# Kernel optimization log

Measured on AMD Instinct MI355X. Metric: run time of the kernel, lower is better.

The kernel has to match this reference:

```python
import jax, jax.numpy as jnp
import numpy as np

N_NODES = 50000
N_EDGES = 800000
N_GRAPHS = 64
IN_DIM, HID_DIM, OUT_DIM = 64, 128, 3


def setup_inputs() -> dict:
    key = jax.random.key(0)
    ks = jax.random.split(key, 8)
    x = jax.random.normal(ks[0], (N_NODES, IN_DIM), dtype=jnp.float32)
    edge_index = jax.random.randint(ks[1], (2, N_EDGES), 0, N_NODES, dtype=jnp.int64)
    batch = jnp.sort(jax.random.randint(ks[2], (N_NODES,), 0, N_GRAPHS, dtype=jnp.int64))
    # Glorot-ish init for weights, zero biases (matches GCNConv/Linear defaults in spirit)
    W1 = jax.random.normal(ks[3], (IN_DIM, HID_DIM), dtype=jnp.float32) / np.sqrt(IN_DIM)
    b1 = jnp.zeros((HID_DIM,), dtype=jnp.float32)
    W2 = jax.random.normal(ks[4], (HID_DIM, HID_DIM), dtype=jnp.float32) / np.sqrt(HID_DIM)
    b2 = jnp.zeros((HID_DIM,), dtype=jnp.float32)
    Wf = jax.random.normal(ks[5], (HID_DIM, OUT_DIM), dtype=jnp.float32) / np.sqrt(HID_DIM)
    bf = jnp.zeros((OUT_DIM,), dtype=jnp.float32)
    return {"x": x, "edge_index": edge_index, "batch": batch,
            "W1": W1, "b1": b1, "W2": W2, "b2": b2, "Wf": Wf, "bf": bf}


def _gcn_conv(x, src, dst, norm, W, b, n_nodes):
    # PyG GCNConv: h = X W; out_i = sum_{j->i} norm_ij * h_j + b
    h = x @ W                                  # [N, D_out]
    msg = h[src] * norm[:, None]               # gather + scale  [E+N, D_out]
    out = jax.ops.segment_sum(msg, dst, num_segments=n_nodes)  # scatter-add
    return out + b


def reference(x, edge_index, batch, W1, b1, W2, b2, Wf, bf):
    n_nodes = x.shape[0]
    loops = jnp.arange(n_nodes, dtype=edge_index.dtype)
    src = jnp.concatenate([edge_index[0], loops])  # add self-loops
    dst = jnp.concatenate([edge_index[1], loops])
    # Symmetric normalization: deg over destinations (incl. self-loops)
    deg = jax.ops.segment_sum(jnp.ones_like(dst, dtype=x.dtype), dst, num_segments=n_nodes)
    dinv = jax.lax.rsqrt(jnp.maximum(deg, 1.0))
    norm = dinv[src] * dinv[dst]               # [E+N]

    h = jax.nn.relu(_gcn_conv(x, src, dst, norm, W1, b1, n_nodes))
    h = jax.nn.relu(_gcn_conv(h, src, dst, norm, W2, b2, n_nodes))

    # global_mean_pool over batch ids
    sums = jax.ops.segment_sum(h, batch, num_segments=N_GRAPHS)        # [G, H]
    counts = jax.ops.segment_sum(jnp.ones((n_nodes,), h.dtype), batch, num_segments=N_GRAPHS)
    pooled = sums / jnp.maximum(counts, 1.0)[:, None]

    return pooled @ Wf + bf                    # [G, OUT_DIM]
```

## Files before the change

kernel.cpp:

```cpp
#include <hip/hip_runtime.h>

constexpr int NN = 50000;
constexpr int NE = 800000;
constexpr int NG = 64;
constexpr int DI = 64;
constexpr int DH = 128;
constexpr int DO = 3;

constexpr int SCAN_B = 256;
constexpr int NBK = 196;
constexpr int CHUNK = 4096;
constexpr int NCH = (NE + CHUNK - 1) / CHUNK;
constexpr int BBTOT = NBK * NCH;
constexpr int NBB = (BBTOT + 255) / 256;

typedef unsigned int u32;

__device__ inline float blo(u32 u) { return __uint_as_float(u << 16); }
__device__ inline float bhi(u32 u) { return __uint_as_float(u & 0xffff0000u); }
__device__ inline u32 f2b(float f) {
    u32 u = __float_as_uint(f);
    return (u + 0x7fffu + ((u >> 16) & 1u)) >> 16;
}
__device__ inline void fma8(float w, uint4 v, float acc[8]) {
    acc[0] = fmaf(w, blo(v.x), acc[0]); acc[1] = fmaf(w, bhi(v.x), acc[1]);
    acc[2] = fmaf(w, blo(v.y), acc[2]); acc[3] = fmaf(w, bhi(v.y), acc[3]);
    acc[4] = fmaf(w, blo(v.z), acc[4]); acc[5] = fmaf(w, bhi(v.z), acc[5]);
    acc[6] = fmaf(w, blo(v.w), acc[6]); acc[7] = fmaf(w, bhi(v.w), acc[7]);
}

__global__ void k_init(const float* __restrict__ x, uint4* __restrict__ xb,
                       float* __restrict__ pooled, const int* __restrict__ batch,
                       int* __restrict__ gstart) {
    int i = blockIdx.x * blockDim.x + threadIdx.x;
    if (i < NN * DI / 8) {
        float4 a = reinterpret_cast<const float4*>(x)[i * 2];
        float4 b = reinterpret_cast<const float4*>(x)[i * 2 + 1];
        uint4 o;
        o.x = f2b(a.x) | (f2b(a.y) << 16);
        o.y = f2b(a.z) | (f2b(a.w) << 16);
        o.z = f2b(b.x) | (f2b(b.y) << 16);
        o.w = f2b(b.z) | (f2b(b.w) << 16);
        xb[i] = o;
    }
    if (i < NG * DH) pooled[i] = 0.0f;
    if (blockIdx.x == 0 && threadIdx.x <= NG) {
        int g = threadIdx.x;
        int lo = 0, hi = NN;
        while (lo < hi) {
            int mid = (lo + hi) >> 1;
            if (batch[mid] < g) lo = mid + 1; else hi = mid;
        }
        gstart[g] = lo;
    }
}

__global__ __launch_bounds__(256) void k_histc(const int* __restrict__ dst,
                                               int* __restrict__ cntBB) {
    __shared__ int lcnt[NBK];
    const int t = threadIdx.x, c = blockIdx.x;
    for (int b = t; b < NBK; b += 256) lcnt[b] = 0;
    __syncthreads();
    const int base = c * CHUNK;
    const int endE = min(base + CHUNK, NE);
    for (int e = base + t; e < endE; e += 256) atomicAdd(&lcnt[dst[e] >> 8], 1);
    __syncthreads();
    for (int b = t; b < NBK; b += 256) cntBB[b * NCH + c] = lcnt[b];
}

__device__ inline void blockScan(int* sm) {
    for (int off = 1; off < SCAN_B; off <<= 1) {
        int add = (threadIdx.x >= off) ? sm[threadIdx.x - off] : 0;
        __syncthreads();
        sm[threadIdx.x] += add;
        __syncthreads();
    }
}

__global__ void k_scanBB1(int* __restrict__ cntBB, int* __restrict__ bbpartial) {
    __shared__ int sm[SCAN_B];
    int i = blockIdx.x * SCAN_B + threadIdx.x;
    int v = (i < BBTOT) ? cntBB[i] : 0;
    sm[threadIdx.x] = v;
    __syncthreads();
    blockScan(sm);
    if (i < BBTOT) cntBB[i] = sm[threadIdx.x] - v;
    if (threadIdx.x == SCAN_B - 1) bbpartial[blockIdx.x] = sm[SCAN_B - 1];
}

__global__ void k_scanB(int* __restrict__ bbpartial) {
    __shared__ int sm[SCAN_B];
    int v = (threadIdx.x < NBB) ? bbpartial[threadIdx.x] : 0;
    sm[threadIdx.x] = v;
    __syncthreads();
    blockScan(sm);
    if (threadIdx.x < NBB) bbpartial[threadIdx.x] = sm[threadIdx.x] - v;
}

__global__ __launch_bounds__(256) void k_fillP2(const int* __restrict__ src,
                                                const int* __restrict__ dst,
                                                const int* __restrict__ cntBB,
                                                const int* __restrict__ bbpartial,
                                                u32* __restrict__ stage) {
    __shared__ int lcur[NBK];
    const int t = threadIdx.x, c = blockIdx.x;
    for (int b = t; b < NBK; b += 256) {
        int i = b * NCH + c;
        lcur[b] = cntBB[i] + bbpartial[i >> 8];
    }
    __syncthreads();
    const int base = c * CHUNK;
    const int endE = min(base + CHUNK, NE);
    for (int e = base + t; e < endE; e += 256) {
        int s = src[e], d = dst[e];
        int slot = atomicAdd(&lcur[d >> 8], 1);
        stage[slot] = ((u32)(d & 255) << 16) | (u32)s;
    }
}

__global__ __launch_bounds__(256) void k_fillB(const u32* __restrict__ stage,
                                               const int* __restrict__ cntBB,
                                               const int* __restrict__ bbpartial,
                                               int* __restrict__ rowptr,
                                               float* __restrict__ dinv,
                                               ushort* __restrict__ csr16) {
    __shared__ int cnt[256];
    __shared__ int sm[256];
    __shared__ int cur[256];
    const int b = blockIdx.x, t = threadIdx.x;
    cnt[t] = 0;
    const int i0 = b * NCH;
    const int beg = cntBB[i0] + bbpartial[i0 >> 8];
    const int end = (b + 1 < NBK) ? cntBB[i0 + NCH] + bbpartial[(i0 + NCH) >> 8] : NE;
    __syncthreads();
    for (int i = beg + t; i < end; i += 256) atomicAdd(&cnt[(stage[i] >> 16) & 255u], 1);
    __syncthreads();
    const int v = cnt[t];
    sm[t] = v;
    __syncthreads();
    blockScan(sm);
    const int excl = sm[t] - v;
    const int n = b * 256 + t;
    if (n < NN) {
        rowptr[n] = beg + excl;
        dinv[n] = rsqrtf((float)(v + 1));
    }
    if (b == NBK - 1 && t == 0) rowptr[NN] = NE;
    cur[t] = beg + excl;
    __syncthreads();
    for (int i = beg + t; i < end; i += 256) {
        u32 e = stage[i];
        int slot = atomicAdd(&cur[(e >> 16) & 255u], 1);
        csr16[slot] = (ushort)(e & 0xffffu);
    }
}

template <int D, bool BIAS_RELU>
__global__ __launch_bounds__(256) void k_agge(const ushort* __restrict__ hb,
                                              const ushort* __restrict__ csr16,
                                              const int* __restrict__ rowptr,
                                              const float* __restrict__ dinv,
                                              const float* __restrict__ bias,
                                              u32* __restrict__ out) {
    constexpr int SUB = D / 8;
    constexpr int NPB = 256 / SUB;
    const int sub = threadIdx.x / SUB;
    const int sl = threadIdx.x % SUB;
    const int node = blockIdx.x * NPB + sub;
    if (node >= NN) return;

    const float dn = dinv[node];
    float acc[8];
    {
        uint4 v = *reinterpret_cast<const uint4*>(hb + (size_t)node * D + sl * 8);
        float w = dn * dn;
        acc[0] = w * blo(v.x); acc[1] = w * bhi(v.x);
        acc[2] = w * blo(v.y); acc[3] = w * bhi(v.y);
        acc[4] = w * blo(v.z); acc[5] = w * bhi(v.z);
        acc[6] = w * blo(v.w); acc[7] = w * bhi(v.w);
    }
    int j = rowptr[node];
    const int end = rowptr[node + 1];
    while ((j & 3) && j < end) {
        int s = csr16[j];
        uint4 g = *reinterpret_cast<const uint4*>(hb + (size_t)s * D + sl * 8);
        fma8(dn * dinv[s], g, acc);
        ++j;
    }
    for (; j + 4 <= end; j += 4) {
        ushort4 q = *reinterpret_cast<const ushort4*>(csr16 + j);
        uint4 g0 = *reinterpret_cast<const uint4*>(hb + (size_t)q.x * D + sl * 8);
        uint4 g1 = *reinterpret_cast<const uint4*>(hb + (size_t)q.y * D + sl * 8);
        uint4 g2 = *reinterpret_cast<const uint4*>(hb + (size_t)q.z * D + sl * 8);
        uint4 g3 = *reinterpret_cast<const uint4*>(hb + (size_t)q.w * D + sl * 8);
        float w0 = dn * dinv[q.x], w1 = dn * dinv[q.y];
        float w2 = dn * dinv[q.z], w3 = dn * dinv[q.w];
        fma8(w0, g0, acc);
        fma8(w1, g1, acc);
        fma8(w2, g2, acc);
        fma8(w3, g3, acc);
    }
    while (j < end) {
        int s = csr16[j];
        uint4 g = *reinterpret_cast<const uint4*>(hb + (size_t)s * D + sl * 8);
        fma8(dn * dinv[s], g, acc);
        ++j;
    }
    if (BIAS_RELU) {
        float4 b0 = *reinterpret_cast<const float4*>(bias + sl * 8);
        float4 b1v = *reinterpret_cast<const float4*>(bias + sl * 8 + 4);
        acc[0] = fmaxf(acc[0] + b0.x, 0.f); acc[1] = fmaxf(acc[1] + b0.y, 0.f);
        acc[2] = fmaxf(acc[2] + b0.z, 0.f); acc[3] = fmaxf(acc[3] + b0.w, 0.f);
        acc[4] = fmaxf(acc[4] + b1v.x, 0.f); acc[5] = fmaxf(acc[5] + b1v.y, 0.f);
        acc[6] = fmaxf(acc[6] + b1v.z, 0.f); acc[7] = fmaxf(acc[7] + b1v.w, 0.f);
    }
    uint4 o;
    o.x = f2b(acc[0]) | (f2b(acc[1]) << 16);
    o.y = f2b(acc[2]) | (f2b(acc[3]) << 16);
    o.z = f2b(acc[4]) | (f2b(acc[5]) << 16);
    o.w = f2b(acc[6]) | (f2b(acc[7]) << 16);
    *reinterpret_cast<uint4*>(reinterpret_cast<ushort*>(out) + (size_t)node * D + sl * 8) = o;
}

__device__ inline float4 fmaf4(float s, float4 w, float4 a) {
    a.x = fmaf(s, w.x, a.x); a.y = fmaf(s, w.y, a.y);
    a.z = fmaf(s, w.z, a.z); a.w = fmaf(s, w.w, a.w);
    return a;
}

constexpr int GR = 32;

__global__ __launch_bounds__(256) void k_gemm12(const ushort* __restrict__ A,
                                                const float* __restrict__ W1,
                                                const float* __restrict__ b1,
                                                const float* __restrict__ W2,
                                                u32* __restrict__ T) {
    constexpr int ASTR = 72;
    __shared__ ushort sU16[GR * DH];
    const int t = threadIdx.x;
    const int row0 = blockIdx.x * GR;
    const int cg = t & 31;
    const int rw = t >> 5;

    {
        const int row = t >> 3;
        const int q = t & 7;
        int gr = row0 + row;
        uint4 v = make_uint4(0u, 0u, 0u, 0u);
        if (gr < NN)
            v = *reinterpret_cast<const uint4*>(A + (size_t)gr * DI + q * 8);
        *reinterpret_cast<uint4*>(&sU16[row * ASTR + q * 8]) = v;
    }
    __syncthreads();

    const float* W1c = W1 + cg * 4;
    float4 acc[4];
#pragma unroll
    for (int j = 0; j < 4; ++j) acc[j] = make_float4(0.f, 0.f, 0.f, 0.f);

#pragma unroll 4
    for (int kk = 0; kk < DI; kk += 4) {
        float4 w0 = *reinterpret_cast<const float4*>(W1c + (kk + 0) * DH);
        float4 w1 = *reinterpret_cast<const float4*>(W1c + (kk + 1) * DH);
        float4 w2 = *reinterpret_cast<const float4*>(W1c + (kk + 2) * DH);
        float4 w3 = *reinterpret_cast<const float4*>(W1c + (kk + 3) * DH);
#pragma unroll
        for (int j = 0; j < 4; ++j) {
            uint2 av = *reinterpret_cast<const uint2*>(&sU16[(rw * 4 + j) * ASTR + kk]);
            acc[j] = fmaf4(blo(av.x), w0, acc[j]);
            acc[j] = fmaf4(bhi(av.x), w1, acc[j]);
            acc[j] = fmaf4(blo(av.y), w2, acc[j]);
            acc[j] = fmaf4(bhi(av.y), w3, acc[j]);
        }
    }
    {
        float4 bb = *reinterpret_cast<const float4*>(b1 + cg * 4);
#pragma unroll
        for (int j = 0; j < 4; ++j) {
            acc[j].x = fmaxf(acc[j].x + bb.x, 0.f);
            acc[j].y = fmaxf(acc[j].y + bb.y, 0.f);
            acc[j].z = fmaxf(acc[j].z + bb.z, 0.f);
            acc[j].w = fmaxf(acc[j].w + bb.w, 0.f);
        }
    }

    __syncthreads();
#pragma unroll
    for (int j = 0; j < 4; ++j) {
        uint2 o = make_uint2(f2b(acc[j].x) | (f2b(acc[j].y) << 16),
                             f2b(acc[j].z) | (f2b(acc[j].w) << 16));
        *reinterpret_cast<uint2*>(&sU16[(rw * 4 + j) * DH + cg * 4]) = o;
    }
    __syncthreads();

    const float* W2c = W2 + cg * 4;
    float4 acc2[4];
#pragma unroll
    for (int j = 0; j < 4; ++j) acc2[j] = make_float4(0.f, 0.f, 0.f, 0.f);

#pragma unroll 4
    for (int kk = 0; kk < DH; kk += 4) {
        float4 w0 = *reinterpret_cast<const float4*>(W2c + (kk + 0) * DH);
        float4 w1 = *reinterpret_cast<const float4*>(W2c + (kk + 1) * DH);
        float4 w2 = *reinterpret_cast<const float4*>(W2c + (kk + 2) * DH);
        float4 w3 = *reinterpret_cast<const float4*>(W2c + (kk + 3) * DH);
#pragma unroll
        for (int j = 0; j < 4; ++j) {
            uint2 av = *reinterpret_cast<const uint2*>(&sU16[(rw * 4 + j) * DH + kk]);
            acc2[j] = fmaf4(blo(av.x), w0, acc2[j]);
            acc2[j] = fmaf4(bhi(av.x), w1, acc2[j]);
            acc2[j] = fmaf4(blo(av.y), w2, acc2[j]);
            acc2[j] = fmaf4(bhi(av.y), w3, acc2[j]);
        }
    }
#pragma unroll
    for (int j = 0; j < 4; ++j) {
        int gr = row0 + rw * 4 + j;
        if (gr < NN) {
            uint2 o = make_uint2(f2b(acc2[j].x) | (f2b(acc2[j].y) << 16),
                                 f2b(acc2[j].z) | (f2b(acc2[j].w) << 16));
            *reinterpret_cast<uint2*>(&T[(size_t)gr * (DH / 2) + cg * 2]) = o;
        }
    }
}

constexpr int POOL_CHUNK = 64;
__global__ __launch_bounds__(256) void k_pool3(const u32* __restrict__ h2b,
                                               const int* __restrict__ batch,
                                               float* __restrict__ pooled) {
    const int c2 = threadIdx.x & 63;
    const int q = threadIdx.x >> 6;
    const int n0 = blockIdx.x * POOL_CHUNK;
    const int nEnd = min(n0 + POOL_CHUNK, NN);
    float a0 = 0.f, a1 = 0.f;
    int gcur = -1;
    for (int n = n0 + q; n < nEnd; n += 4) {
        int g = batch[n];
        if (g != gcur) {
            if (gcur >= 0) {
                atomicAdd(&pooled[gcur * DH + c2 * 2], a0);
                atomicAdd(&pooled[gcur * DH + c2 * 2 + 1], a1);
            }
            a0 = a1 = 0.f;
            gcur = g;
        }
        u32 v = h2b[(size_t)n * (DH / 2) + c2];
        a0 += blo(v);
        a1 += bhi(v);
    }
    if (gcur >= 0) {
        atomicAdd(&pooled[gcur * DH + c2 * 2], a0);
        atomicAdd(&pooled[gcur * DH + c2 * 2 + 1], a1);
    }
}

__global__ void k_head(const float* __restrict__ pooled, const int* __restrict__ gstart,
                       const float* __restrict__ Wf, const float* __restrict__ bf,
                       float* __restrict__ out) {
    int t = threadIdx.x;
    if (t >= NG * DO) return;
    int g = t / DO, o = t - g * DO;
    float acc = 0.0f;
    for (int k = 0; k < DH; ++k) acc += pooled[g * DH + k] * Wf[k * DO + o];
    float cnt = fmaxf((float)(gstart[g + 1] - gstart[g]), 1.0f);
    out[t] = acc / cnt + bf[o];
}

extern "C" void kernel_launch(void* const* d_in, const int* in_sizes, int n_in,
                              void* d_out, int out_size, void* d_ws, size_t ws_size,
                              hipStream_t stream) {
    const float* x   = (const float*)d_in[0];
    const int* ei    = (const int*)d_in[1];
    const int* batch = (const int*)d_in[2];
    const float* W1  = (const float*)d_in[3];
    const float* b1  = (const float*)d_in[4];
    const float* W2  = (const float*)d_in[5];
    const float* b2  = (const float*)d_in[6];
    const float* Wf  = (const float*)d_in[7];
    const float* bf  = (const float*)d_in[8];
    float* out = (float*)d_out;

    const int* src = ei;
    const int* dst = ei + NE;

    int* rowptr    = (int*)d_ws;
    int* bbpartial = rowptr + 50056;
    int* gstart    = bbpartial + 256;
    int* cntBB     = gstart + 80;
    ushort* csr16  = (ushort*)(cntBB + 38416);
    float* dinv    = (float*)((u32*)(cntBB + 38416) + 400000);
    u32* xbu       = (u32*)(dinv + 50048);
    u32* stage     = xbu + 1600000;
    u32* agg1bu    = stage + 800000;
    u32* tbu       = agg1bu + 1600000;
    u32* h2b       = tbu + 3200000;
    float* pooled  = (float*)(h2b + 3200000);

    ushort* xb    = (ushort*)xbu;
    ushort* agg1b = (ushort*)agg1bu;
    ushort* tb    = (ushort*)tbu;

    const int B = 256;
    k_init<<<(NN * DI / 8 + B - 1) / B, B, 0, stream>>>(x, (uint4*)xb, pooled, batch, gstart);
    k_histc<<<NCH, 256, 0, stream>>>(dst, cntBB);
    k_scanBB1<<<NBB, SCAN_B, 0, stream>>>(cntBB, bbpartial);
    k_scanB<<<1, SCAN_B, 0, stream>>>(bbpartial);
    k_fillP2<<<NCH, 256, 0, stream>>>(src, dst, cntBB, bbpartial, stage);
    k_fillB<<<NBK, 256, 0, stream>>>(stage, cntBB, bbpartial, rowptr, dinv, csr16);

    k_agge<DI, false><<<(NN + 31) / 32, 256, 0, stream>>>(xb, csr16, rowptr, dinv,
                                                          nullptr, agg1bu);
    k_gemm12<<<(NN + GR - 1) / GR, 256, 0, stream>>>(agg1b, W1, b1, W2, tbu);

    k_agge<DH, true><<<(NN + 15) / 16, 256, 0, stream>>>(tb, csr16, rowptr, dinv, b2, h2b);

    k_pool3<<<(NN + POOL_CHUNK - 1) / POOL_CHUNK, 256, 0, stream>>>(h2b, batch, pooled);
    k_head<<<1, 256, 0, stream>>>(pooled, gstart, Wf, bf, out);
}
```

Before: 171.5 us.

## Use bf16 MFMA matrix cores for fused two-layer GEMM

Replaces the scalar-FMA fused GEMM (agg1·W1 + bias + ReLU, then ·W2) with a kernel built on 16x16x32 bf16 MFMA instructions, one wave per 16 rows. W1 and W2 are converted to transposed bf16 copies inside the init kernel so B fragments load straight from global memory. The intermediate activation stays in per-wave LDS. This adds bf16 rounding of the weights, which slightly lowers precision, and the output stores are scalar 16-bit writes.

```diff
diff --git a/kernel.cpp b/kernel.cpp
--- a/kernel.cpp
+++ b/kernel.cpp
@@ -15,6 +15,8 @@
 constexpr int NBB = (BBTOT + 255) / 256;
 
 typedef unsigned int u32;
+typedef __attribute__((ext_vector_type(8))) short bf16x8;
+typedef __attribute__((ext_vector_type(4))) float f32x4;
 
 __device__ inline float blo(u32 u) { return __uint_as_float(u << 16); }
 __device__ inline float bhi(u32 u) { return __uint_as_float(u & 0xffff0000u); }
@@ -31,7 +33,9 @@
 
 __global__ void k_init(const float* __restrict__ x, uint4* __restrict__ xb,
                        float* __restrict__ pooled, const int* __restrict__ batch,
-                       int* __restrict__ gstart) {
+                       int* __restrict__ gstart, const float* __restrict__ W1,
+                       const float* __restrict__ W2, ushort* __restrict__ w1bt,
+                       ushort* __restrict__ w2bt) {
     int i = blockIdx.x * blockDim.x + threadIdx.x;
     if (i < NN * DI / 8) {
         float4 a = reinterpret_cast<const float4*>(x)[i * 2];
@@ -44,6 +48,8 @@
         xb[i] = o;
     }
     if (i < NG * DH) pooled[i] = 0.0f;
+    if (i < DH * DI) w1bt[i] = (ushort)f2b(W1[(i & (DI - 1)) * DH + (i >> 6)]);
+    if (i < DH * DH) w2bt[i] = (ushort)f2b(W2[(i & (DH - 1)) * DH + (i >> 7)]);
     if (blockIdx.x == 0 && threadIdx.x <= NG) {
         int g = threadIdx.x;
         int lo = 0, hi = NN;
@@ -222,104 +228,68 @@
     *reinterpret_cast<uint4*>(reinterpret_cast<ushort*>(out) + (size_t)node * D + sl * 8) = o;
 }
 
-__device__ inline float4 fmaf4(float s, float4 w, float4 a) {
-    a.x = fmaf(s, w.x, a.x); a.y = fmaf(s, w.y, a.y);
-    a.z = fmaf(s, w.z, a.z); a.w = fmaf(s, w.w, a.w);
-    return a;
-}
-
-constexpr int GR = 32;
-
-__global__ __launch_bounds__(256) void k_gemm12(const ushort* __restrict__ A,
-                                                const float* __restrict__ W1,
-                                                const float* __restrict__ b1,
-                                                const float* __restrict__ W2,
-                                                u32* __restrict__ T) {
-    constexpr int ASTR = 72;
-    __shared__ ushort sU16[GR * DH];
+__global__ __launch_bounds__(256) void k_gemm12m(const ushort* __restrict__ A,
+                                                 const ushort* __restrict__ w1bt,
+                                                 const float* __restrict__ b1,
+                                                 const ushort* __restrict__ w2bt,
+                                                 ushort* __restrict__ T) {
+    constexpr int HP = 136;
+    __shared__ ushort sH[4 * 16 * HP];
     const int t = threadIdx.x;
-    const int row0 = blockIdx.x * GR;
-    const int cg = t & 31;
-    const int rw = t >> 5;
-
+    const int w = t >> 6;
+    const int l = t & 63;
+    const int r16 = l & 15;
+    const int kg = l >> 4;
+    const int row0 = blockIdx.x * 64 + w * 16;
+    ushort* sHw = &sH[w * 16 * HP];
+
+    bf16x8 a1_0, a1_1;
     {
-        const int row = t >> 3;
-        const int q = t & 7;
-        int gr = row0 + row;
-        uint4 v = make_uint4(0u, 0u, 0u, 0u);
-        if (gr < NN)
-            v = *reinterpret_cast<const uint4*>(A + (size_t)gr * DI + q * 8);
-        *reinterpret_cast<uint4*>(&sU16[row * ASTR + q * 8]) = v;
-    }
-    __syncthreads();
-
-    const float* W1c = W1 + cg * 4;
-    float4 acc[4];
+        int gr = row0 + r16;
+        const ushort* Ap = A + (size_t)(gr < NN ? gr : NN - 1) * DI + kg * 8;
+        a1_0 = *reinterpret_cast<const bf16x8*>(Ap);
+        a1_1 = *reinterpret_cast<const bf16x8*>(Ap + 32);
+    }
+
 #pragma unroll
-    for (int j = 0; j < 4; ++j) acc[j] = make_float4(0.f, 0.f, 0.f, 0.f);
-
-#pragma unroll 4
-    for (int kk = 0; kk < DI; kk += 4) {
-        float4 w0 = *reinterpret_cast<const float4*>(W1c + (kk + 0) * DH);
-        float4 w1 = *reinterpret_cast<const float4*>(W1c + (kk + 1) * DH);
-        float4 w2 = *reinterpret_cast<const float4*>(W1c + (kk + 2) * DH);
-        float4 w3 = *reinterpret_cast<const float4*>(W1c + (kk + 3) * DH);
+    for (int ct = 0; ct < 8; ++ct) {
+        const ushort* Bp = w1bt + (size_t)(ct * 16 + r16) * DI + kg * 8;
+        bf16x8 b0 = *reinterpret_cast<const bf16x8*>(Bp);
+        bf16x8 bq = *reinterpret_cast<const bf16x8*>(Bp + 32);
+        f32x4 c = {0.f, 0.f, 0.f, 0.f};
+        c = __builtin_amdgcn_mfma_f32_16x16x32_bf16(a1_0, b0, c, 0, 0, 0);
+        c = __builtin_amdgcn_mfma_f32_16x16x32_bf16(a1_1, bq, c, 0, 0, 0);
+        float bb = b1[ct * 16 + r16];
 #pragma unroll
-        for (int j = 0; j < 4; ++j) {
-            uint2 av = *reinterpret_cast<const uint2*>(&sU16[(rw * 4 + j) * ASTR + kk]);
-            acc[j] = fmaf4(blo(av.x), w0, acc[j]);
-            acc[j] = fmaf4(bhi(av.x), w1, acc[j]);
-            acc[j] = fmaf4(blo(av.y), w2, acc[j]);
-            acc[j] = fmaf4(bhi(av.y), w3, acc[j]);
+        for (int r = 0; r < 4; ++r) {
+            float v = fmaxf(c[r] + bb, 0.f);
+            sHw[(kg * 4 + r) * HP + ct * 16 + r16] = (ushort)f2b(v);
         }
     }
-    {
-        float4 bb = *reinterpret_cast<const float4*>(b1 + cg * 4);
+    __syncthreads();
+
+    bf16x8 a2_0 = *reinterpret_cast<const bf16x8*>(&sHw[r16 * HP + 0 * 32 + kg * 8]);
+    bf16x8 a2_1 = *reinterpret_cast<const bf16x8*>(&sHw[r16 * HP + 1 * 32 + kg * 8]);
+    bf16x8 a2_2 = *reinterpret_cast<const bf16x8*>(&sHw[r16 * HP + 2 * 32 + kg * 8]);
+    bf16x8 a2_3 = *reinterpret_cast<const bf16x8*>(&sHw[r16 * HP + 3 * 32 + kg * 8]);
+
 #pragma unroll
-        for (int j = 0; j < 4; ++j) {
-            acc[j].x = fmaxf(acc[j].x + bb.x, 0.f);
-            acc[j].y = fmaxf(acc[j].y + bb.y, 0.f);
-            acc[j].z = fmaxf(acc[j].z + bb.z, 0.f);
-            acc[j].w = fmaxf(acc[j].w + bb.w, 0.f);
-        }
-    }
-
-    __syncthreads();
+    for (int ct = 0; ct < 8; ++ct) {
+        const ushort* Bp = w2bt + (size_t)(ct * 16 + r16) * DH + kg * 8;
+        bf16x8 b0 = *reinterpret_cast<const bf16x8*>(Bp);
+        bf16x8 b1v = *reinterpret_cast<const bf16x8*>(Bp + 32);
+        bf16x8 b2v = *reinterpret_cast<const bf16x8*>(Bp + 64);
+        bf16x8 b3v = *reinterpret_cast<const bf16x8*>(Bp + 96);
+        f32x4 c = {0.f, 0.f, 0.f, 0.f};
+        c = __builtin_amdgcn_mfma_f32_16x16x32_bf16(a2_0, b0, c, 0, 0, 0);
+        c = __builtin_amdgcn_mfma_f32_16x16x32_bf16(a2_1, b1v, c, 0, 0, 0);
+        c = __builtin_amdgcn_mfma_f32_16x16x32_bf16(a2_2, b2v, c, 0, 0, 0);
+        c = __builtin_amdgcn_mfma_f32_16x16x32_bf16(a2_3, b3v, c, 0, 0, 0);
 #pragma unroll
-    for (int j = 0; j < 4; ++j) {
-        uint2 o = make_uint2(f2b(acc[j].x) | (f2b(acc[j].y) << 16),
-                             f2b(acc[j].z) | (f2b(acc[j].w) << 16));
-        *reinterpret_cast<uint2*>(&sU16[(rw * 4 + j) * DH + cg * 4]) = o;
-    }
-    __syncthreads();
-
-    const float* W2c = W2 + cg * 4;
-    float4 acc2[4];
-#pragma unroll
-    for (int j = 0; j < 4; ++j) acc2[j] = make_float4(0.f, 0.f, 0.f, 0.f);
-
-#pragma unroll 4
-    for (int kk = 0; kk < DH; kk += 4) {
-        float4 w0 = *reinterpret_cast<const float4*>(W2c + (kk + 0) * DH);
-        float4 w1 = *reinterpret_cast<const float4*>(W2c + (kk + 1) * DH);
-        float4 w2 = *reinterpret_cast<const float4*>(W2c + (kk + 2) * DH);
-        float4 w3 = *reinterpret_cast<const float4*>(W2c + (kk + 3) * DH);
-#pragma unroll
-        for (int j = 0; j < 4; ++j) {
-            uint2 av = *reinterpret_cast<const uint2*>(&sU16[(rw * 4 + j) * DH + kk]);
-            acc2[j] = fmaf4(blo(av.x), w0, acc2[j]);
-            acc2[j] = fmaf4(bhi(av.x), w1, acc2[j]);
-            acc2[j] = fmaf4(blo(av.y), w2, acc2[j]);
-            acc2[j] = fmaf4(bhi(av.y), w3, acc2[j]);
-        }
-    }
-#pragma unroll
-    for (int j = 0; j < 4; ++j) {
-        int gr = row0 + rw * 4 + j;
-        if (gr < NN) {
-            uint2 o = make_uint2(f2b(acc2[j].x) | (f2b(acc2[j].y) << 16),
-                                 f2b(acc2[j].z) | (f2b(acc2[j].w) << 16));
-            *reinterpret_cast<uint2*>(&T[(size_t)gr * (DH / 2) + cg * 2]) = o;
+        for (int r = 0; r < 4; ++r) {
+            int gr = row0 + kg * 4 + r;
+            if (gr < NN)
+                T[(size_t)gr * DH + ct * 16 + r16] = (ushort)f2b(c[r]);
         }
     }
 }
@@ -395,13 +365,16 @@
     u32* tbu       = agg1bu + 1600000;
     u32* h2b       = tbu + 3200000;
     float* pooled  = (float*)(h2b + 3200000);
+    ushort* w1bt   = (ushort*)(pooled + 8192);
+    ushort* w2bt   = w1bt + 8192;
 
     ushort* xb    = (ushort*)xbu;
     ushort* agg1b = (ushort*)agg1bu;
     ushort* tb    = (ushort*)tbu;
 
     const int B = 256;
-    k_init<<<(NN * DI / 8 + B - 1) / B, B, 0, stream>>>(x, (uint4*)xb, pooled, batch, gstart);
+    k_init<<<(NN * DI / 8 + B - 1) / B, B, 0, stream>>>(x, (uint4*)xb, pooled, batch,
+                                                        gstart, W1, W2, w1bt, w2bt);
     k_histc<<<NCH, 256, 0, stream>>>(dst, cntBB);
     k_scanBB1<<<NBB, SCAN_B, 0, stream>>>(cntBB, bbpartial);
     k_scanB<<<1, SCAN_B, 0, stream>>>(bbpartial);
@@ -410,7 +383,7 @@
 
     k_agge<DI, false><<<(NN + 31) / 32, 256, 0, stream>>>(xb, csr16, rowptr, dinv,
                                                           nullptr, agg1bu);
-    k_gemm12<<<(NN + GR - 1) / GR, 256, 0, stream>>>(agg1b, W1, b1, W2, tbu);
+    k_gemm12m<<<(NN + 63) / 64, 256, 0, stream>>>(agg1b, w1bt, b1, w2bt, tb);
 
     k_agge<DH, true><<<(NN + 15) / 16, 256, 0, stream>>>(tb, csr16, rowptr, dinv, b2, h2b);
 
```

Result: faster. 150.2 us (-12.4%).
